# Optimization experiments

Measured on AMD Instinct MI355X. Metric: run time of the kernel, lower is better.

The kernel has to match this reference:

```python
import jax, jax.numpy as jnp
import numpy as np

BN_EPS = 1e-5


def setup_inputs() -> dict:
    key = jax.random.key(0)
    ks = jax.random.split(key, 10)
    B, C, L = 16, 512, 1024
    scale = 1.0 / np.sqrt(C)
    inp = {
        "x": jax.random.normal(ks[0], (B, C, L), dtype=jnp.float32),
        "gamma": jnp.ones((C,), jnp.float32),
        "beta": jnp.zeros((C,), jnp.float32),
        "Wq": jax.random.normal(ks[1], (C, C), jnp.float32) * scale,
        "bq": jnp.zeros((C,), jnp.float32),
        "Wk": jax.random.normal(ks[2], (C, C), jnp.float32) * scale,
        "bk": jnp.zeros((C,), jnp.float32),
        "Wv": jax.random.normal(ks[3], (C, C), jnp.float32) * scale,
        "bv": jnp.zeros((C,), jnp.float32),
        "Wp": jax.random.normal(ks[4], (C, C), jnp.float32) * scale,
        "bp": jnp.zeros((C,), jnp.float32),
    }
    return inp


def _pointwise(W, b, h):
    # Conv1d with kernel_size=1 == per-position linear: [C_out,C_in] x [B,C_in,L]
    return jnp.einsum("oc,bcl->bol", W, h) + b[None, :, None]


def reference(x, gamma, beta, Wq, bq, Wk, bk, Wv, bv, Wp, bp):
    B, C, L = x.shape
    # BatchNorm1d (training-mode batch statistics over batch & length dims)
    mean = jnp.mean(x, axis=(0, 2), keepdims=True)
    var = jnp.var(x, axis=(0, 2), keepdims=True)
    hn = (x - mean) * jax.lax.rsqrt(var + BN_EPS)
    hn = hn * gamma[None, :, None] + beta[None, :, None]

    q = _pointwise(Wq, bq, hn)  # [B,C,L]
    k = _pointwise(Wk, bk, hn)
    v = _pointwise(Wv, bv, hn)

    # attn[b,i,j] = sum_c q[b,c,i] k[b,c,j] / sqrt(C); i=query pos, j=key pos
    attn = jnp.einsum("bci,bcj->bij", q, k) * (C ** -0.5)
    attn = jax.nn.softmax(attn, axis=-1)

    # out[b,c,i] = sum_j attn[b,i,j] v[b,c,j]
    h_ = jnp.einsum("bij,bcj->bci", attn, v)
    h_ = _pointwise(Wp, bp, h_)
    return x + h_
```

## Files before the change

kernel.cpp:

```cpp
#include <hip/hip_runtime.h>
#include <hip/hip_bf16.h>


#define BB 16
#define CC 512
#define LL 1024

typedef __bf16 bf16x8 __attribute__((ext_vector_type(8)));
typedef float  f32x4  __attribute__((ext_vector_type(4)));

__device__ inline unsigned short bf16_bits(float f) {
  __hip_bfloat16 h = __float2bfloat16(f);
  return __builtin_bit_cast(unsigned short, h);
}
__device__ inline float bits_lo(unsigned int u) {
  return __builtin_bit_cast(float, u << 16);
}
__device__ inline float bits_hi(unsigned int u) {
  return __builtin_bit_cast(float, u & 0xffff0000u);
}

__global__ __launch_bounds__(256) void bn_stats(
    const float* __restrict__ x, const float* __restrict__ gamma,
    const float* __restrict__ beta, float* __restrict__ scl,
    float* __restrict__ sft) {
  int c = blockIdx.x;
  int t = threadIdx.x;
  float s = 0.f, s2 = 0.f;
  for (int b = 0; b < BB; ++b) {
    float4 v = ((const float4*)(x + ((size_t)(b * CC + c)) * LL))[t];
    s  += v.x + v.y + v.z + v.w;
    s2 += v.x * v.x + v.y * v.y + v.z * v.z + v.w * v.w;
  }
  for (int m = 32; m; m >>= 1) { s += __shfl_xor(s, m, 64); s2 += __shfl_xor(s2, m, 64); }
  __shared__ float rs[4], rs2[4];
  int wave = t >> 6, lane = t & 63;
  if (lane == 0) { rs[wave] = s; rs2[wave] = s2; }
  __syncthreads();
  if (t == 0) {
    float S  = rs[0] + rs[1] + rs[2] + rs[3];
    float S2 = rs2[0] + rs2[1] + rs2[2] + rs2[3];
    float mean = S * (1.f / 16384.f);
    float var  = S2 * (1.f / 16384.f) - mean * mean;
    float sc = gamma[c] * rsqrtf(var + 1e-5f);
    scl[c] = sc;
    sft[c] = beta[c] - mean * sc;
  }
}

__global__ __launch_bounds__(256) void cast4(
    const float* __restrict__ Wq, const float* __restrict__ Wk,
    const float* __restrict__ Wv, const float* __restrict__ Wp,
    __hip_bfloat16* __restrict__ Wqkv, __hip_bfloat16* __restrict__ Wpb) {
  int m = blockIdx.y;
  const float* src = m == 0 ? Wq : m == 1 ? Wk : m == 2 ? Wv : Wp;
  __hip_bfloat16* dst = m < 3 ? Wqkv + (size_t)m * 262144 : Wpb;
  int i = blockIdx.x * 256 + threadIdx.x;
  float4 v = ((const float4*)src)[i];
  ushort4 o;
  o.x = bf16_bits(v.x); o.y = bf16_bits(v.y);
  o.z = bf16_bits(v.z); o.w = bf16_bits(v.w);
  ((ushort4*)dst)[i] = o;
}

__global__ __launch_bounds__(256) void norm_t(
    const float* __restrict__ x, const float* __restrict__ scl,
    const float* __restrict__ sft, __hip_bfloat16* __restrict__ hnT) {
  __shared__ float tile[32][33];
  int l0 = blockIdx.x * 32, c0 = blockIdx.y * 32, b = blockIdx.z;
  int t = threadIdx.x;
#pragma unroll
  for (int i = 0; i < 4; ++i) {
    int idx = t + i * 256;
    int cc = idx >> 5, ll = idx & 31;
    tile[cc][ll] = x[((size_t)(b * CC + c0 + cc)) * LL + l0 + ll];
  }
  __syncthreads();
#pragma unroll
  for (int i = 0; i < 2; ++i) {
    int idx = t + i * 256;
    int ll = idx >> 4, cc = (idx & 15) * 2;
    float v0 = tile[cc][ll] * scl[c0 + cc] + sft[c0 + cc];
    float v1 = tile[cc + 1][ll] * scl[c0 + cc + 1] + sft[c0 + cc + 1];
    ushort2 o; o.x = bf16_bits(v0); o.y = bf16_bits(v1);
    *(ushort2*)(hnT + ((size_t)(b * LL + l0 + ll)) * CC + c0 + cc) = o;
  }
}

__global__ __launch_bounds__(256) void softmax_bf16(__hip_bfloat16* __restrict__ S) {
  int wave = threadIdx.x >> 6, lane = threadIdx.x & 63;
  size_t row = (size_t)blockIdx.x * 4 + wave;
  uint4* p = (uint4*)(S + row * 1024);
  uint4 r0 = p[lane * 2], r1 = p[lane * 2 + 1];
  float f[16];
  unsigned int w[8] = {r0.x, r0.y, r0.z, r0.w, r1.x, r1.y, r1.z, r1.w};
#pragma unroll
  for (int i = 0; i < 8; ++i) { f[2 * i] = bits_lo(w[i]); f[2 * i + 1] = bits_hi(w[i]); }
  float mx = f[0];
#pragma unroll
  for (int i = 1; i < 16; ++i) mx = fmaxf(mx, f[i]);
  for (int m = 32; m; m >>= 1) mx = fmaxf(mx, __shfl_xor(mx, m, 64));
  float s = 0.f;
#pragma unroll
  for (int i = 0; i < 16; ++i) { f[i] = __expf(f[i] - mx); s += f[i]; }
  for (int m = 32; m; m >>= 1) s += __shfl_xor(s, m, 64);
  float inv = 1.f / s;
  unsigned int ow[8];
#pragma unroll
  for (int i = 0; i < 8; ++i) {
    unsigned int lo = bf16_bits(f[2 * i] * inv);
    unsigned int hi = bf16_bits(f[2 * i + 1] * inv);
    ow[i] = lo | (hi << 16);
  }
  uint4 o0 = {ow[0], ow[1], ow[2], ow[3]}, o1 = {ow[4], ow[5], ow[6], ow[7]};
  p[lane * 2] = o0; p[lane * 2 + 1] = o1;
}

__device__ __forceinline__ void gemm_core(
    const __hip_bfloat16* __restrict__ A, int lda,
    const __hip_bfloat16* __restrict__ B, int ldb, int K,
    __hip_bfloat16* sA, __hip_bfloat16* sB, f32x4 (&acc)[4][4]) {
  const int tid = threadIdx.x;
  const int wave = tid >> 6, lane = tid & 63;
  const int wm = (wave >> 1) * 64, wn = (wave & 1) * 64;
  const int row0 = tid >> 2;
  const int ke0 = (((tid & 3) ^ ((tid >> 3) & 3)) * 8);
  const int fr = lane & 15;
  const int q = lane >> 4;
  const int colA = ((q ^ ((fr >> 1) & 3)) * 8);
  for (int k0 = 0; k0 < K; k0 += 32) {
    __syncthreads();
#pragma unroll
    for (int it = 0; it < 2; ++it) {
      const __hip_bfloat16* ga = A + (size_t)(it * 64 + row0) * lda + (k0 + ke0);
      const __hip_bfloat16* gb = B + (size_t)(it * 64 + row0) * ldb + (k0 + ke0);
      __builtin_amdgcn_global_load_lds(
          (__attribute__((address_space(1))) void*)(void*)ga,
          (__attribute__((address_space(3))) void*)(sA + (it * 256 + wave * 64) * 8),
          16, 0, 0);
      __builtin_amdgcn_global_load_lds(
          (__attribute__((address_space(1))) void*)(void*)gb,
          (__attribute__((address_space(3))) void*)(sB + (it * 256 + wave * 64) * 8),
          16, 0, 0);
    }
    __syncthreads();
    bf16x8 af[4], bfr[4];
#pragma unroll
    for (int i = 0; i < 4; ++i) {
      af[i]  = *(const bf16x8*)(sA + (wm + i * 16 + fr) * 32 + colA);
      bfr[i] = *(const bf16x8*)(sB + (wn + i * 16 + fr) * 32 + colA);
    }
#pragma unroll
    for (int i = 0; i < 4; ++i)
#pragma unroll
      for (int j = 0; j < 4; ++j)
        acc[i][j] = __builtin_amdgcn_mfma_f32_16x16x32_bf16(af[i], bfr[j], acc[i][j], 0, 0, 0);
  }
}

__global__ __launch_bounds__(256, 3) void gemm_qkv(
    const __hip_bfloat16* __restrict__ Wb, const __hip_bfloat16* __restrict__ hnT,
    __hip_bfloat16* __restrict__ qT, __hip_bfloat16* __restrict__ kT,
    __hip_bfloat16* __restrict__ vN,
    const float* __restrict__ bq, const float* __restrict__ bk,
    const float* __restrict__ bv) {
  __shared__ __align__(16) __hip_bfloat16 sA[128 * 32];
  __shared__ __align__(16) __hip_bfloat16 sB[128 * 32];
  const int bat = blockIdx.z;
  const int m0 = blockIdx.y * 128, n0 = blockIdx.x * 128;
  f32x4 acc[4][4] = {};
  gemm_core(Wb + (size_t)m0 * 512, 512,
            hnT + (size_t)bat * LL * CC + (size_t)n0 * 512, 512, 512, sA, sB, acc);
  const int lane = threadIdx.x & 63, wave = threadIdx.x >> 6;
  const int wm = (wave >> 1) * 64, wn = (wave & 1) * 64;
  const int crow = (lane >> 4) * 4, ccol = lane & 15;
  const int id = m0 >> 9;
  const int mloc0 = m0 & 511;
  const float* bias = id == 0 ? bq : id == 1 ? bk : bv;
  if (id < 2) {
    __hip_bfloat16* D = (id == 0 ? qT : kT) + (size_t)bat * LL * CC;
#pragma unroll
    for (int i = 0; i < 4; ++i) {
      int mg = mloc0 + wm + i * 16 + crow;
      float bv4[4];
#pragma unroll
      for (int r = 0; r < 4; ++r) bv4[r] = bias[mg + r];
#pragma unroll
      for (int j = 0; j < 4; ++j) {
        int ng = n0 + wn + j * 16 + ccol;
        ushort4 o;
        o.x = bf16_bits(acc[i][j][0] + bv4[0]);
        o.y = bf16_bits(acc[i][j][1] + bv4[1]);
        o.z = bf16_bits(acc[i][j][2] + bv4[2]);
        o.w = bf16_bits(acc[i][j][3] + bv4[3]);
        *(ushort4*)(D + (size_t)ng * 512 + mg) = o;
      }
    }
  } else {
    __hip_bfloat16* D = vN + (size_t)bat * CC * LL;
#pragma unroll
    for (int i = 0; i < 4; ++i) {
      int mg = mloc0 + wm + i * 16 + crow;
      float bv4[4];
#pragma unroll
      for (int r = 0; r < 4; ++r) bv4[r] = bias[mg + r];
#pragma unroll
      for (int j = 0; j < 4; ++j) {
        int ng = n0 + wn + j * 16 + ccol;
#pragma unroll
        for (int r = 0; r < 4; ++r)
          D[(size_t)(mg + r) * 1024 + ng] = __float2bfloat16(acc[i][j][r] + bv4[r]);
      }
    }
  }
}

template <int MODE, bool BIAS>
__global__ __launch_bounds__(256, 3) void gemm_tn(
    const __hip_bfloat16* __restrict__ A, int lda, size_t strideA,
    const __hip_bfloat16* __restrict__ B, int ldb, size_t strideB,
    void* __restrict__ Dp, int ldd, size_t strideD,
    const float* __restrict__ bias, float scale,
    const float* __restrict__ resid, size_t strideR, int K) {
  __shared__ __align__(16) __hip_bfloat16 sA[128 * 32];
  __shared__ __align__(16) __hip_bfloat16 sB[128 * 32];
  const int bat = blockIdx.z;
  const int m0 = blockIdx.y * 128, n0 = blockIdx.x * 128;
  f32x4 acc[4][4] = {};
  gemm_core(A + (size_t)bat * strideA + (size_t)m0 * lda, lda,
            B + (size_t)bat * strideB + (size_t)n0 * ldb, ldb, K, sA, sB, acc);
  const int lane = threadIdx.x & 63, wave = threadIdx.x >> 6;
  const int wm = (wave >> 1) * 64, wn = (wave & 1) * 64;
  const int crow = (lane >> 4) * 4, ccol = lane & 15;
  if constexpr (MODE == 0) {
    __hip_bfloat16* D = (__hip_bfloat16*)Dp + (size_t)bat * strideD;
#pragma unroll
    for (int i = 0; i < 4; ++i) {
      int mg = m0 + wm + i * 16 + crow;
      float bv4[4];
#pragma unroll
      for (int r = 0; r < 4; ++r) bv4[r] = BIAS ? bias[mg + r] : 0.f;
#pragma unroll
      for (int j = 0; j < 4; ++j) {
        int ng = n0 + wn + j * 16 + ccol;
#pragma unroll
        for (int r = 0; r < 4; ++r)
          D[(size_t)(mg + r) * ldd + ng] =
              __float2bfloat16(acc[i][j][r] * scale + bv4[r]);
      }
    }
  } else {
    float* D = (float*)Dp + (size_t)bat * strideD;
#pragma unroll
    for (int i = 0; i < 4; ++i) {
      int mg = m0 + wm + i * 16 + crow;
      float bv4[4];
#pragma unroll
      for (int r = 0; r < 4; ++r) bv4[r] = BIAS ? bias[mg + r] : 0.f;
#pragma unroll
      for (int j = 0; j < 4; ++j) {
        int ng = n0 + wn + j * 16 + ccol;
        const float* rsrc = resid + (size_t)bat * strideR + (size_t)mg * ldd + ng;
        float* dst = D + (size_t)mg * ldd + ng;
#pragma unroll
        for (int r = 0; r < 4; ++r)
          dst[(size_t)r * ldd] = acc[i][j][r] * scale + bv4[r] + rsrc[(size_t)r * ldd];
      }
    }
  }
}

extern "C" void kernel_launch(void* const* d_in, const int* in_sizes, int n_in,
                              void* d_out, int out_size, void* d_ws, size_t ws_size,
                              hipStream_t stream) {
  const float* x     = (const float*)d_in[0];
  const float* gamma = (const float*)d_in[1];
  const float* beta  = (const float*)d_in[2];
  const float* Wq    = (const float*)d_in[3];
  const float* bq    = (const float*)d_in[4];
  const float* Wk    = (const float*)d_in[5];
  const float* bk    = (const float*)d_in[6];
  const float* Wv    = (const float*)d_in[7];
  const float* bv    = (const float*)d_in[8];
  const float* Wp    = (const float*)d_in[9];
  const float* bp    = (const float*)d_in[10];
  float* out = (float*)d_out;

  char* ws = (char*)d_ws;
  float* scl = (float*)ws;
  float* sft = scl + 512;
  __hip_bfloat16* Wqkvb = (__hip_bfloat16*)(ws + 4096);
  __hip_bfloat16* Wpb = Wqkvb + 786432;
  __hip_bfloat16* hnT = Wpb + 262144;
  __hip_bfloat16* qT  = hnT + 8388608;
  __hip_bfloat16* kT  = qT + 8388608;
  __hip_bfloat16* vN  = kT + 8388608;
  __hip_bfloat16* Sb  = vN + 8388608;
  __hip_bfloat16* HT  = hnT;

  bn_stats<<<512, 256, 0, stream>>>(x, gamma, beta, scl, sft);
  cast4<<<dim3(256, 4), 256, 0, stream>>>(Wq, Wk, Wv, Wp, Wqkvb, Wpb);
  norm_t<<<dim3(32, 16, 16), 256, 0, stream>>>(x, scl, sft, hnT);

  const size_t sLC = (size_t)LL * CC;
  const size_t sCL = (size_t)CC * LL;
  const size_t sLLb = (size_t)LL * LL;

  gemm_qkv<<<dim3(8, 12, 16), 256, 0, stream>>>(Wqkvb, hnT, qT, kT, vN, bq, bk, bv);
  gemm_tn<0, false><<<dim3(8, 8, 16), 256, 0, stream>>>(
      qT, 512, sLC, kT, 512, sLC, Sb, 1024, sLLb, nullptr,
      0.04419417382415922f, nullptr, 0, 512);
  softmax_bf16<<<4096, 256, 0, stream>>>(Sb);
  gemm_tn<0, false><<<dim3(4, 8, 16), 256, 0, stream>>>(
      Sb, 1024, sLLb, vN, 1024, sCL, HT, 512, sLC, nullptr, 1.f, nullptr, 0, 1024);
  gemm_tn<3, true><<<dim3(8, 4, 16), 256, 0, stream>>>(
      Wpb, 512, 0, HT, 512, sLC, out, 1024, sCL, bp, 1.f, x, sCL, 512);
}
```

Before: 244.2 us.

## Triple-buffer GEMM LDS loads and swap operands for vectorized transposed epilogues

The shared GEMM core now uses a three-stage LDS ring buffer. Loads for tile k+2 are issued while tile k is computed, and partial vmcnt waits replace the two full barriers per K step. This hides global-load latency. The GEMMs also swap A/B operand roles (V projection, scores as K·Q, PV and output projection transposed) so every epilogue writes packed 4-wide bf16 or float4 vectors instead of scattered scalar stores. This costs 48KB of LDS per block, which may cut occupancy below the requested three blocks per CU, and the qkv kernel is split into separate qk and v launches.

```diff
diff --git a/kernel.cpp b/kernel.cpp
--- a/kernel.cpp
+++ b/kernel.cpp
@@ -51,10 +51,11 @@
 __global__ __launch_bounds__(256) void cast4(
     const float* __restrict__ Wq, const float* __restrict__ Wk,
     const float* __restrict__ Wv, const float* __restrict__ Wp,
-    __hip_bfloat16* __restrict__ Wqkv, __hip_bfloat16* __restrict__ Wpb) {
+    __hip_bfloat16* __restrict__ Wqk, __hip_bfloat16* __restrict__ Wvb,
+    __hip_bfloat16* __restrict__ Wpb) {
   int m = blockIdx.y;
   const float* src = m == 0 ? Wq : m == 1 ? Wk : m == 2 ? Wv : Wp;
-  __hip_bfloat16* dst = m < 3 ? Wqkv + (size_t)m * 262144 : Wpb;
+  __hip_bfloat16* dst = m == 0 ? Wqk : m == 1 ? Wqk + 262144 : m == 2 ? Wvb : Wpb;
   int i = blockIdx.x * 256 + threadIdx.x;
   float4 v = ((const float4*)src)[i];
   ushort4 o;
@@ -116,10 +117,16 @@
   p[lane * 2] = o0; p[lane * 2 + 1] = o1;
 }
 
+__device__ inline void glds(const __hip_bfloat16* g, __hip_bfloat16* l) {
+  __builtin_amdgcn_global_load_lds(
+      (__attribute__((address_space(1))) void*)(void*)g,
+      (__attribute__((address_space(3))) void*)l, 16, 0, 0);
+}
+
 __device__ __forceinline__ void gemm_core(
     const __hip_bfloat16* __restrict__ A, int lda,
     const __hip_bfloat16* __restrict__ B, int ldb, int K,
-    __hip_bfloat16* sA, __hip_bfloat16* sB, f32x4 (&acc)[4][4]) {
+    __hip_bfloat16* sm, f32x4 (&acc)[4][4]) {
   const int tid = threadIdx.x;
   const int wave = tid >> 6, lane = tid & 63;
   const int wm = (wave >> 1) * 64, wn = (wave & 1) * 64;
@@ -128,144 +135,147 @@
   const int fr = lane & 15;
   const int q = lane >> 4;
   const int colA = ((q ^ ((fr >> 1) & 3)) * 8);
-  for (int k0 = 0; k0 < K; k0 += 32) {
-    __syncthreads();
-#pragma unroll
-    for (int it = 0; it < 2; ++it) {
-      const __hip_bfloat16* ga = A + (size_t)(it * 64 + row0) * lda + (k0 + ke0);
-      const __hip_bfloat16* gb = B + (size_t)(it * 64 + row0) * ldb + (k0 + ke0);
-      __builtin_amdgcn_global_load_lds(
-          (__attribute__((address_space(1))) void*)(void*)ga,
-          (__attribute__((address_space(3))) void*)(sA + (it * 256 + wave * 64) * 8),
-          16, 0, 0);
-      __builtin_amdgcn_global_load_lds(
-          (__attribute__((address_space(1))) void*)(void*)gb,
-          (__attribute__((address_space(3))) void*)(sB + (it * 256 + wave * 64) * 8),
-          16, 0, 0);
-    }
-    __syncthreads();
+  const int dofs = wave * 512;
+
+  const __hip_bfloat16* ga0 = A + (size_t)row0 * lda + ke0;
+  const __hip_bfloat16* ga1 = ga0 + (size_t)64 * lda;
+  const __hip_bfloat16* gb0 = B + (size_t)row0 * ldb + ke0;
+  const __hip_bfloat16* gb1 = gb0 + (size_t)64 * ldb;
+
+  __hip_bfloat16* rb = sm;
+  __hip_bfloat16* nb = sm + 8192;
+  __hip_bfloat16* wb = sm + 16384;
+
+  const int niters = K >> 5;
+  {
+    glds(ga0, rb + dofs);          glds(ga1, rb + 2048 + dofs);
+    glds(gb0, rb + 4096 + dofs);   glds(gb1, rb + 6144 + dofs);
+    glds(ga0 + 32, nb + dofs);        glds(ga1 + 32, nb + 2048 + dofs);
+    glds(gb0 + 32, nb + 4096 + dofs); glds(gb1 + 32, nb + 6144 + dofs);
+  }
+  for (int k = 0; k < niters; ++k) {
+    if (k + 1 < niters) __builtin_amdgcn_s_waitcnt(0x0F74);
+    else                __builtin_amdgcn_s_waitcnt(0x0F70);
+    __builtin_amdgcn_s_barrier();
+    if (k + 2 < niters) {
+      int ko = (k + 2) * 32;
+      glds(ga0 + ko, wb + dofs);          glds(ga1 + ko, wb + 2048 + dofs);
+      glds(gb0 + ko, wb + 4096 + dofs);   glds(gb1 + ko, wb + 6144 + dofs);
+    }
     bf16x8 af[4], bfr[4];
 #pragma unroll
     for (int i = 0; i < 4; ++i) {
-      af[i]  = *(const bf16x8*)(sA + (wm + i * 16 + fr) * 32 + colA);
-      bfr[i] = *(const bf16x8*)(sB + (wn + i * 16 + fr) * 32 + colA);
+      af[i]  = *(const bf16x8*)(rb + (wm + i * 16 + fr) * 32 + colA);
+      bfr[i] = *(const bf16x8*)(rb + 4096 + (wn + i * 16 + fr) * 32 + colA);
     }
 #pragma unroll
     for (int i = 0; i < 4; ++i)
 #pragma unroll
       for (int j = 0; j < 4; ++j)
         acc[i][j] = __builtin_amdgcn_mfma_f32_16x16x32_bf16(af[i], bfr[j], acc[i][j], 0, 0, 0);
-  }
-}
-
-__global__ __launch_bounds__(256, 3) void gemm_qkv(
+    __hip_bfloat16* t = rb; rb = nb; nb = wb; wb = t;
+  }
+}
+
+__global__ __launch_bounds__(256, 3) void gemm_qk(
     const __hip_bfloat16* __restrict__ Wb, const __hip_bfloat16* __restrict__ hnT,
     __hip_bfloat16* __restrict__ qT, __hip_bfloat16* __restrict__ kT,
-    __hip_bfloat16* __restrict__ vN,
-    const float* __restrict__ bq, const float* __restrict__ bk,
-    const float* __restrict__ bv) {
-  __shared__ __align__(16) __hip_bfloat16 sA[128 * 32];
-  __shared__ __align__(16) __hip_bfloat16 sB[128 * 32];
+    const float* __restrict__ bq, const float* __restrict__ bk) {
+  __shared__ __align__(16) __hip_bfloat16 sm[3 * 8192];
   const int bat = blockIdx.z;
   const int m0 = blockIdx.y * 128, n0 = blockIdx.x * 128;
   f32x4 acc[4][4] = {};
   gemm_core(Wb + (size_t)m0 * 512, 512,
-            hnT + (size_t)bat * LL * CC + (size_t)n0 * 512, 512, 512, sA, sB, acc);
+            hnT + (size_t)bat * LL * CC + (size_t)n0 * 512, 512, 512, sm, acc);
   const int lane = threadIdx.x & 63, wave = threadIdx.x >> 6;
   const int wm = (wave >> 1) * 64, wn = (wave & 1) * 64;
   const int crow = (lane >> 4) * 4, ccol = lane & 15;
   const int id = m0 >> 9;
   const int mloc0 = m0 & 511;
-  const float* bias = id == 0 ? bq : id == 1 ? bk : bv;
-  if (id < 2) {
-    __hip_bfloat16* D = (id == 0 ? qT : kT) + (size_t)bat * LL * CC;
-#pragma unroll
-    for (int i = 0; i < 4; ++i) {
-      int mg = mloc0 + wm + i * 16 + crow;
-      float bv4[4];
-#pragma unroll
-      for (int r = 0; r < 4; ++r) bv4[r] = bias[mg + r];
-#pragma unroll
-      for (int j = 0; j < 4; ++j) {
-        int ng = n0 + wn + j * 16 + ccol;
-        ushort4 o;
-        o.x = bf16_bits(acc[i][j][0] + bv4[0]);
-        o.y = bf16_bits(acc[i][j][1] + bv4[1]);
-        o.z = bf16_bits(acc[i][j][2] + bv4[2]);
-        o.w = bf16_bits(acc[i][j][3] + bv4[3]);
-        *(ushort4*)(D + (size_t)ng * 512 + mg) = o;
-      }
-    }
-  } else {
-    __hip_bfloat16* D = vN + (size_t)bat * CC * LL;
-#pragma unroll
-    for (int i = 0; i < 4; ++i) {
-      int mg = mloc0 + wm + i * 16 + crow;
-      float bv4[4];
-#pragma unroll
-      for (int r = 0; r < 4; ++r) bv4[r] = bias[mg + r];
-#pragma unroll
-      for (int j = 0; j < 4; ++j) {
-        int ng = n0 + wn + j * 16 + ccol;
-#pragma unroll
-        for (int r = 0; r < 4; ++r)
-          D[(size_t)(mg + r) * 1024 + ng] = __float2bfloat16(acc[i][j][r] + bv4[r]);
-      }
-    }
-  }
-}
-
-template <int MODE, bool BIAS>
-__global__ __launch_bounds__(256, 3) void gemm_tn(
+  const float* bias = id == 0 ? bq : bk;
+  __hip_bfloat16* D = (id == 0 ? qT : kT) + (size_t)bat * LL * CC;
+#pragma unroll
+  for (int i = 0; i < 4; ++i) {
+    int mg = mloc0 + wm + i * 16 + crow;
+    float bv4[4];
+#pragma unroll
+    for (int r = 0; r < 4; ++r) bv4[r] = bias[mg + r];
+#pragma unroll
+    for (int j = 0; j < 4; ++j) {
+      int ng = n0 + wn + j * 16 + ccol;
+      ushort4 o;
+      o.x = bf16_bits(acc[i][j][0] + bv4[0]);
+      o.y = bf16_bits(acc[i][j][1] + bv4[1]);
+      o.z = bf16_bits(acc[i][j][2] + bv4[2]);
+      o.w = bf16_bits(acc[i][j][3] + bv4[3]);
+      *(ushort4*)(D + (size_t)ng * 512 + mg) = o;
+    }
+  }
+}
+
+template <bool BIAS>
+__global__ __launch_bounds__(256, 3) void gemm_bf16t(
     const __hip_bfloat16* __restrict__ A, int lda, size_t strideA,
     const __hip_bfloat16* __restrict__ B, int ldb, size_t strideB,
-    void* __restrict__ Dp, int ldd, size_t strideD,
-    const float* __restrict__ bias, float scale,
-    const float* __restrict__ resid, size_t strideR, int K) {
-  __shared__ __align__(16) __hip_bfloat16 sA[128 * 32];
-  __shared__ __align__(16) __hip_bfloat16 sB[128 * 32];
+    __hip_bfloat16* __restrict__ D, int ldd, size_t strideD,
+    const float* __restrict__ bias, float scale, int K) {
+  __shared__ __align__(16) __hip_bfloat16 sm[3 * 8192];
   const int bat = blockIdx.z;
   const int m0 = blockIdx.y * 128, n0 = blockIdx.x * 128;
   f32x4 acc[4][4] = {};
   gemm_core(A + (size_t)bat * strideA + (size_t)m0 * lda, lda,
-            B + (size_t)bat * strideB + (size_t)n0 * ldb, ldb, K, sA, sB, acc);
+            B + (size_t)bat * strideB + (size_t)n0 * ldb, ldb, K, sm, acc);
   const int lane = threadIdx.x & 63, wave = threadIdx.x >> 6;
   const int wm = (wave >> 1) * 64, wn = (wave & 1) * 64;
   const int crow = (lane >> 4) * 4, ccol = lane & 15;
-  if constexpr (MODE == 0) {
-    __hip_bfloat16* D = (__hip_bfloat16*)Dp + (size_t)bat * strideD;
+  __hip_bfloat16* Db = D + (size_t)bat * strideD;
+#pragma unroll
+  for (int j = 0; j < 4; ++j) {
+    int ng = n0 + wn + j * 16 + ccol;
+    float bn = BIAS ? bias[ng] : 0.f;
 #pragma unroll
     for (int i = 0; i < 4; ++i) {
       int mg = m0 + wm + i * 16 + crow;
-      float bv4[4];
-#pragma unroll
-      for (int r = 0; r < 4; ++r) bv4[r] = BIAS ? bias[mg + r] : 0.f;
-#pragma unroll
-      for (int j = 0; j < 4; ++j) {
-        int ng = n0 + wn + j * 16 + ccol;
-#pragma unroll
-        for (int r = 0; r < 4; ++r)
-          D[(size_t)(mg + r) * ldd + ng] =
-              __float2bfloat16(acc[i][j][r] * scale + bv4[r]);
-      }
-    }
-  } else {
-    float* D = (float*)Dp + (size_t)bat * strideD;
+      ushort4 o;
+      o.x = bf16_bits(acc[i][j][0] * scale + bn);
+      o.y = bf16_bits(acc[i][j][1] * scale + bn);
+      o.z = bf16_bits(acc[i][j][2] * scale + bn);
+      o.w = bf16_bits(acc[i][j][3] * scale + bn);
+      *(ushort4*)(Db + (size_t)ng * ldd + mg) = o;
+    }
+  }
+}
+
+__global__ __launch_bounds__(256, 3) void gemm_f32t(
+    const __hip_bfloat16* __restrict__ A, int lda, size_t strideA,
+    const __hip_bfloat16* __restrict__ B, int ldb,
+    float* __restrict__ D, int ldd, size_t strideD,
+    const float* __restrict__ bias, const float* __restrict__ resid, int K) {
+  __shared__ __align__(16) __hip_bfloat16 sm[3 * 8192];
+  const int bat = blockIdx.z;
+  const int m0 = blockIdx.y * 128, n0 = blockIdx.x * 128;
+  f32x4 acc[4][4] = {};
+  gemm_core(A + (size_t)bat * strideA + (size_t)m0 * lda, lda,
+            B + (size_t)n0 * ldb, ldb, K, sm, acc);
+  const int lane = threadIdx.x & 63, wave = threadIdx.x >> 6;
+  const int wm = (wave >> 1) * 64, wn = (wave & 1) * 64;
+  const int crow = (lane >> 4) * 4, ccol = lane & 15;
+  float* Db = D + (size_t)bat * strideD;
+  const float* Rb = resid + (size_t)bat * strideD;
+#pragma unroll
+  for (int j = 0; j < 4; ++j) {
+    int ng = n0 + wn + j * 16 + ccol;
+    float bn = bias[ng];
 #pragma unroll
     for (int i = 0; i < 4; ++i) {
       int mg = m0 + wm + i * 16 + crow;
-      float bv4[4];
-#pragma unroll
-      for (int r = 0; r < 4; ++r) bv4[r] = BIAS ? bias[mg + r] : 0.f;
-#pragma unroll
-      for (int j = 0; j < 4; ++j) {
-        int ng = n0 + wn + j * 16 + ccol;
-        const float* rsrc = resid + (size_t)bat * strideR + (size_t)mg * ldd + ng;
-        float* dst = D + (size_t)mg * ldd + ng;
-#pragma unroll
-        for (int r = 0; r < 4; ++r)
-          dst[(size_t)r * ldd] = acc[i][j][r] * scale + bv4[r] + rsrc[(size_t)r * ldd];
-      }
+      float4 r = *(const float4*)(Rb + (size_t)ng * ldd + mg);
+      float4 o;
+      o.x = acc[i][j][0] + bn + r.x;
+      o.y = acc[i][j][1] + bn + r.y;
+      o.z = acc[i][j][2] + bn + r.z;
+      o.w = acc[i][j][3] + bn + r.w;
+      *(float4*)(Db + (size_t)ng * ldd + mg) = o;
     }
   }
 }
@@ -289,30 +299,33 @@
   char* ws = (char*)d_ws;
   float* scl = (float*)ws;
   float* sft = scl + 512;
-  __hip_bfloat16* Wqkvb = (__hip_bfloat16*)(ws + 4096);
-  __hip_bfloat16* Wpb = Wqkvb + 786432;
-  __hip_bfloat16* hnT = Wpb + 262144;
-  __hip_bfloat16* qT  = hnT + 8388608;
-  __hip_bfloat16* kT  = qT + 8388608;
-  __hip_bfloat16* vN  = kT + 8388608;
-  __hip_bfloat16* Sb  = vN + 8388608;
-  __hip_bfloat16* HT  = hnT;
-
-  bn_stats<<<512, 256, 0, stream>>>(x, gamma, beta, scl, sft);
-  cast4<<<dim3(256, 4), 256, 0, stream>>>(Wq, Wk, Wv, Wp, Wqkvb, Wpb);
-  norm_t<<<dim3(32, 16, 16), 256, 0, stream>>>(x, scl, sft, hnT);
+  __hip_bfloat16* Wqkb = (__hip_bfloat16*)(ws + 4096);
+  __hip_bfloat16* Wvb  = Wqkb + 524288;
+  __hip_bfloat16* Wpb  = Wvb + 262144;
+  __hip_bfloat16* hnT  = Wpb + 262144;
+  __hip_bfloat16* qT   = hnT + 8388608;
+  __hip_bfloat16* kT   = qT + 8388608;
+  __hip_bfloat16* vN   = kT + 8388608;
+  __hip_bfloat16* Sb   = vN + 8388608;
+  __hip_bfloat16* HT   = hnT;
 
   const size_t sLC = (size_t)LL * CC;
   const size_t sCL = (size_t)CC * LL;
   const size_t sLLb = (size_t)LL * LL;
 
-  gemm_qkv<<<dim3(8, 12, 16), 256, 0, stream>>>(Wqkvb, hnT, qT, kT, vN, bq, bk, bv);
-  gemm_tn<0, false><<<dim3(8, 8, 16), 256, 0, stream>>>(
-      qT, 512, sLC, kT, 512, sLC, Sb, 1024, sLLb, nullptr,
-      0.04419417382415922f, nullptr, 0, 512);
+  bn_stats<<<512, 256, 0, stream>>>(x, gamma, beta, scl, sft);
+  cast4<<<dim3(256, 4), 256, 0, stream>>>(Wq, Wk, Wv, Wp, Wqkb, Wvb, Wpb);
+  norm_t<<<dim3(32, 16, 16), 256, 0, stream>>>(x, scl, sft, hnT);
+
+  gemm_qk<<<dim3(8, 8, 16), 256, 0, stream>>>(Wqkb, hnT, qT, kT, bq, bk);
+  gemm_bf16t<true><<<dim3(4, 8, 16), 256, 0, stream>>>(
+      hnT, 512, sLC, Wvb, 512, 0, vN, 1024, sCL, bv, 1.f, 512);
+  gemm_bf16t<false><<<dim3(8, 8, 16), 256, 0, stream>>>(
+      kT, 512, sLC, qT, 512, sLC, Sb, 1024, sLLb, nullptr,
+      0.04419417382415922f, 512);
   softmax_bf16<<<4096, 256, 0, stream>>>(Sb);
-  gemm_tn<0, false><<<dim3(4, 8, 16), 256, 0, stream>>>(
-      Sb, 1024, sLLb, vN, 1024, sCL, HT, 512, sLC, nullptr, 1.f, nullptr, 0, 1024);
-  gemm_tn<3, true><<<dim3(8, 4, 16), 256, 0, stream>>>(
-      Wpb, 512, 0, HT, 512, sLC, out, 1024, sCL, bp, 1.f, x, sCL, 512);
-}
+  gemm_bf16t<false><<<dim3(8, 4, 16), 256, 0, stream>>>(
+      vN, 1024, sCL, Sb, 1024, sLLb, HT, 512, sLC, nullptr, 1.f, 1024);
+  gemm_f32t<<<dim3(4, 8, 16), 256, 0, stream>>>(
+      HT, 512, sLC, Wpb, 512, out, 1024, sCL, bp, x, 512);
+}
```

Measured after the change: 254.5 us. 1.04x slower.

## Fuse softmax normalization into PV GEMM and transpose epilogues for vector stores

Applied to the files above, without the earlier changes.

The softmax pass now only computes per-row max and inverse sum and writes them to a small stats buffer, instead of rewriting the full score matrix. The P·V GEMM recomputes exp(s-max)*inv on the fly while loading score tiles, which removes one full read-write of the score matrix. The S and output-projection GEMMs swap operand roles so epilogues write 4-wide vectorized stores along the contiguous dimension. The cost is extra exp work inside the GEMM inner loop, repeated for each of the four channel tiles.

```diff
diff --git a/kernel.cpp b/kernel.cpp
--- a/kernel.cpp
+++ b/kernel.cpp
@@ -87,10 +87,11 @@
   }
 }
 
-__global__ __launch_bounds__(256) void softmax_bf16(__hip_bfloat16* __restrict__ S) {
+__global__ __launch_bounds__(256) void row_stats(
+    const __hip_bfloat16* __restrict__ S, float2* __restrict__ st) {
   int wave = threadIdx.x >> 6, lane = threadIdx.x & 63;
   size_t row = (size_t)blockIdx.x * 4 + wave;
-  uint4* p = (uint4*)(S + row * 1024);
+  const uint4* p = (const uint4*)(S + row * 1024);
   uint4 r0 = p[lane * 2], r1 = p[lane * 2 + 1];
   float f[16];
   unsigned int w[8] = {r0.x, r0.y, r0.z, r0.w, r1.x, r1.y, r1.z, r1.w};
@@ -102,18 +103,15 @@
   for (int m = 32; m; m >>= 1) mx = fmaxf(mx, __shfl_xor(mx, m, 64));
   float s = 0.f;
 #pragma unroll
-  for (int i = 0; i < 16; ++i) { f[i] = __expf(f[i] - mx); s += f[i]; }
+  for (int i = 0; i < 16; ++i) s += __expf(f[i] - mx);
   for (int m = 32; m; m >>= 1) s += __shfl_xor(s, m, 64);
-  float inv = 1.f / s;
-  unsigned int ow[8];
-#pragma unroll
-  for (int i = 0; i < 8; ++i) {
-    unsigned int lo = bf16_bits(f[2 * i] * inv);
-    unsigned int hi = bf16_bits(f[2 * i + 1] * inv);
-    ow[i] = lo | (hi << 16);
-  }
-  uint4 o0 = {ow[0], ow[1], ow[2], ow[3]}, o1 = {ow[4], ow[5], ow[6], ow[7]};
-  p[lane * 2] = o0; p[lane * 2 + 1] = o1;
+  if (lane == 0) st[row] = make_float2(mx, 1.f / s);
+}
+
+__device__ inline void glds(const __hip_bfloat16* g, __hip_bfloat16* l) {
+  __builtin_amdgcn_global_load_lds(
+      (__attribute__((address_space(1))) void*)(void*)g,
+      (__attribute__((address_space(3))) void*)l, 16, 0, 0);
 }
 
 __device__ __forceinline__ void gemm_core(
@@ -134,14 +132,8 @@
     for (int it = 0; it < 2; ++it) {
       const __hip_bfloat16* ga = A + (size_t)(it * 64 + row0) * lda + (k0 + ke0);
       const __hip_bfloat16* gb = B + (size_t)(it * 64 + row0) * ldb + (k0 + ke0);
-      __builtin_amdgcn_global_load_lds(
-          (__attribute__((address_space(1))) void*)(void*)ga,
-          (__attribute__((address_space(3))) void*)(sA + (it * 256 + wave * 64) * 8),
-          16, 0, 0);
-      __builtin_amdgcn_global_load_lds(
-          (__attribute__((address_space(1))) void*)(void*)gb,
-          (__attribute__((address_space(3))) void*)(sB + (it * 256 + wave * 64) * 8),
-          16, 0, 0);
+      glds(ga, sA + (it * 256 + wave * 64) * 8);
+      glds(gb, sB + (it * 256 + wave * 64) * 8);
     }
     __syncthreads();
     bf16x8 af[4], bfr[4];
@@ -215,57 +207,142 @@
   }
 }
 
-template <int MODE, bool BIAS>
-__global__ __launch_bounds__(256, 3) void gemm_tn(
+__global__ __launch_bounds__(256, 3) void gemm_s(
+    const __hip_bfloat16* __restrict__ kT, const __hip_bfloat16* __restrict__ qT,
+    __hip_bfloat16* __restrict__ Sb) {
+  __shared__ __align__(16) __hip_bfloat16 sA[128 * 32];
+  __shared__ __align__(16) __hip_bfloat16 sB[128 * 32];
+  const int bat = blockIdx.z;
+  const int m0 = blockIdx.y * 128, n0 = blockIdx.x * 128;
+  f32x4 acc[4][4] = {};
+  const size_t sLC = (size_t)LL * CC;
+  gemm_core(kT + (size_t)bat * sLC + (size_t)m0 * 512, 512,
+            qT + (size_t)bat * sLC + (size_t)n0 * 512, 512, 512, sA, sB, acc);
+  const int lane = threadIdx.x & 63, wave = threadIdx.x >> 6;
+  const int wm = (wave >> 1) * 64, wn = (wave & 1) * 64;
+  const int crow = (lane >> 4) * 4, ccol = lane & 15;
+  const float scale = 0.04419417382415922f;
+  __hip_bfloat16* Db = Sb + (size_t)bat * LL * LL;
+#pragma unroll
+  for (int j = 0; j < 4; ++j) {
+    int ng = n0 + wn + j * 16 + ccol;
+#pragma unroll
+    for (int i = 0; i < 4; ++i) {
+      int mg = m0 + wm + i * 16 + crow;
+      ushort4 o;
+      o.x = bf16_bits(acc[i][j][0] * scale);
+      o.y = bf16_bits(acc[i][j][1] * scale);
+      o.z = bf16_bits(acc[i][j][2] * scale);
+      o.w = bf16_bits(acc[i][j][3] * scale);
+      *(ushort4*)(Db + (size_t)ng * 1024 + mg) = o;
+    }
+  }
+}
+
+__global__ __launch_bounds__(256, 3) void attn_pv(
+    const __hip_bfloat16* __restrict__ vN, const __hip_bfloat16* __restrict__ Sb,
+    const float2* __restrict__ st, __hip_bfloat16* __restrict__ HT) {
+  __shared__ __align__(16) __hip_bfloat16 sA[128 * 32];
+  __shared__ __align__(16) __hip_bfloat16 sB[128 * 32];
+  __shared__ float sM[128], sLi[128];
+  const int bat = blockIdx.z;
+  const int m0 = blockIdx.y * 128;
+  const int n0 = blockIdx.x * 128;
+  const int tid = threadIdx.x;
+  if (tid < 128) {
+    float2 s = st[(size_t)bat * LL + n0 + tid];
+    sM[tid] = s.x; sLi[tid] = s.y;
+  }
+  const __hip_bfloat16* A = vN + (size_t)bat * CC * LL + (size_t)m0 * 1024;
+  const __hip_bfloat16* B = Sb + (size_t)bat * LL * LL + (size_t)n0 * 1024;
+  const int wave = tid >> 6, lane = tid & 63;
+  const int wm = (wave >> 1) * 64, wn = (wave & 1) * 64;
+  const int row0 = tid >> 2;
+  const int ke0 = (((tid & 3) ^ ((tid >> 3) & 3)) * 8);
+  const int fr = lane & 15;
+  const int q = lane >> 4;
+  const int colA = ((q ^ ((fr >> 1) & 3)) * 8);
+  f32x4 acc[4][4] = {};
+  for (int k0 = 0; k0 < 1024; k0 += 32) {
+    __syncthreads();
+#pragma unroll
+    for (int it = 0; it < 2; ++it) {
+      glds(A + (size_t)(it * 64 + row0) * 1024 + (k0 + ke0),
+           sA + (it * 256 + wave * 64) * 8);
+      glds(B + (size_t)(it * 64 + row0) * 1024 + (k0 + ke0),
+           sB + (it * 256 + wave * 64) * 8);
+    }
+    __syncthreads();
+    bf16x8 af[4], bfr[4];
+#pragma unroll
+    for (int i = 0; i < 4; ++i)
+      af[i] = *(const bf16x8*)(sA + (wm + i * 16 + fr) * 32 + colA);
+#pragma unroll
+    for (int j = 0; j < 4; ++j) {
+      int rrow = wn + j * 16 + fr;
+      float mrow = sM[rrow], li = sLi[rrow];
+      bf16x8 raw = *(const bf16x8*)(sB + rrow * 32 + colA);
+      bf16x8 p;
+#pragma unroll
+      for (int e = 0; e < 8; ++e)
+        p[e] = (__bf16)(__expf((float)raw[e] - mrow) * li);
+      bfr[j] = p;
+    }
+#pragma unroll
+    for (int i = 0; i < 4; ++i)
+#pragma unroll
+      for (int j = 0; j < 4; ++j)
+        acc[i][j] = __builtin_amdgcn_mfma_f32_16x16x32_bf16(af[i], bfr[j], acc[i][j], 0, 0, 0);
+  }
+  const int crow = (lane >> 4) * 4, ccol = lane & 15;
+  __hip_bfloat16* Db = HT + (size_t)bat * LL * CC;
+#pragma unroll
+  for (int j = 0; j < 4; ++j) {
+    int ng = n0 + wn + j * 16 + ccol;
+#pragma unroll
+    for (int i = 0; i < 4; ++i) {
+      int mg = m0 + wm + i * 16 + crow;
+      ushort4 o;
+      o.x = bf16_bits(acc[i][j][0]);
+      o.y = bf16_bits(acc[i][j][1]);
+      o.z = bf16_bits(acc[i][j][2]);
+      o.w = bf16_bits(acc[i][j][3]);
+      *(ushort4*)(Db + (size_t)ng * 512 + mg) = o;
+    }
+  }
+}
+
+__global__ __launch_bounds__(256, 3) void gemm_f32t(
     const __hip_bfloat16* __restrict__ A, int lda, size_t strideA,
-    const __hip_bfloat16* __restrict__ B, int ldb, size_t strideB,
-    void* __restrict__ Dp, int ldd, size_t strideD,
-    const float* __restrict__ bias, float scale,
-    const float* __restrict__ resid, size_t strideR, int K) {
+    const __hip_bfloat16* __restrict__ B, int ldb,
+    float* __restrict__ D, int ldd, size_t strideD,
+    const float* __restrict__ bias, const float* __restrict__ resid, int K) {
   __shared__ __align__(16) __hip_bfloat16 sA[128 * 32];
   __shared__ __align__(16) __hip_bfloat16 sB[128 * 32];
   const int bat = blockIdx.z;
   const int m0 = blockIdx.y * 128, n0 = blockIdx.x * 128;
   f32x4 acc[4][4] = {};
   gemm_core(A + (size_t)bat * strideA + (size_t)m0 * lda, lda,
-            B + (size_t)bat * strideB + (size_t)n0 * ldb, ldb, K, sA, sB, acc);
+            B + (size_t)n0 * ldb, ldb, K, sA, sB, acc);
   const int lane = threadIdx.x & 63, wave = threadIdx.x >> 6;
   const int wm = (wave >> 1) * 64, wn = (wave & 1) * 64;
   const int crow = (lane >> 4) * 4, ccol = lane & 15;
-  if constexpr (MODE == 0) {
-    __hip_bfloat16* D = (__hip_bfloat16*)Dp + (size_t)bat * strideD;
+  float* Db = D + (size_t)bat * strideD;
+  const float* Rb = resid + (size_t)bat * strideD;
+#pragma unroll
+  for (int j = 0; j < 4; ++j) {
+    int ng = n0 + wn + j * 16 + ccol;
+    float bn = bias[ng];
 #pragma unroll
     for (int i = 0; i < 4; ++i) {
       int mg = m0 + wm + i * 16 + crow;
-      float bv4[4];
-#pragma unroll
-      for (int r = 0; r < 4; ++r) bv4[r] = BIAS ? bias[mg + r] : 0.f;
-#pragma unroll
-      for (int j = 0; j < 4; ++j) {
-        int ng = n0 + wn + j * 16 + ccol;
-#pragma unroll
-        for (int r = 0; r < 4; ++r)
-          D[(size_t)(mg + r) * ldd + ng] =
-              __float2bfloat16(acc[i][j][r] * scale + bv4[r]);
-      }
-    }
-  } else {
-    float* D = (float*)Dp + (size_t)bat * strideD;
-#pragma unroll
-    for (int i = 0; i < 4; ++i) {
-      int mg = m0 + wm + i * 16 + crow;
-      float bv4[4];
-#pragma unroll
-      for (int r = 0; r < 4; ++r) bv4[r] = BIAS ? bias[mg + r] : 0.f;
-#pragma unroll
-      for (int j = 0; j < 4; ++j) {
-        int ng = n0 + wn + j * 16 + ccol;
-        const float* rsrc = resid + (size_t)bat * strideR + (size_t)mg * ldd + ng;
-        float* dst = D + (size_t)mg * ldd + ng;
-#pragma unroll
-        for (int r = 0; r < 4; ++r)
-          dst[(size_t)r * ldd] = acc[i][j][r] * scale + bv4[r] + rsrc[(size_t)r * ldd];
-      }
+      float4 r = *(const float4*)(Rb + (size_t)ng * ldd + mg);
+      float4 o;
+      o.x = acc[i][j][0] + bn + r.x;
+      o.y = acc[i][j][1] + bn + r.y;
+      o.z = acc[i][j][2] + bn + r.z;
+      o.w = acc[i][j][3] + bn + r.w;
+      *(float4*)(Db + (size_t)ng * ldd + mg) = o;
     }
   }
 }
@@ -290,29 +367,26 @@
   float* scl = (float*)ws;
   float* sft = scl + 512;
   __hip_bfloat16* Wqkvb = (__hip_bfloat16*)(ws + 4096);
-  __hip_bfloat16* Wpb = Wqkvb + 786432;
-  __hip_bfloat16* hnT = Wpb + 262144;
-  __hip_bfloat16* qT  = hnT + 8388608;
-  __hip_bfloat16* kT  = qT + 8388608;
-  __hip_bfloat16* vN  = kT + 8388608;
-  __hip_bfloat16* Sb  = vN + 8388608;
-  __hip_bfloat16* HT  = hnT;
+  __hip_bfloat16* Wpb  = Wqkvb + 786432;
+  __hip_bfloat16* hnT  = Wpb + 262144;
+  __hip_bfloat16* qT   = hnT + 8388608;
+  __hip_bfloat16* kT   = qT + 8388608;
+  __hip_bfloat16* vN   = kT + 8388608;
+  __hip_bfloat16* Sb   = vN + 8388608;
+  float2* stats = (float2*)(Sb + 16777216);
+  __hip_bfloat16* HT   = hnT;
+
+  const size_t sLC = (size_t)LL * CC;
+  const size_t sCL = (size_t)CC * LL;
 
   bn_stats<<<512, 256, 0, stream>>>(x, gamma, beta, scl, sft);
   cast4<<<dim3(256, 4), 256, 0, stream>>>(Wq, Wk, Wv, Wp, Wqkvb, Wpb);
   norm_t<<<dim3(32, 16, 16), 256, 0, stream>>>(x, scl, sft, hnT);
 
-  const size_t sLC = (size_t)LL * CC;
-  const size_t sCL = (size_t)CC * LL;
-  const size_t sLLb = (size_t)LL * LL;
-
   gemm_qkv<<<dim3(8, 12, 16), 256, 0, stream>>>(Wqkvb, hnT, qT, kT, vN, bq, bk, bv);
-  gemm_tn<0, false><<<dim3(8, 8, 16), 256, 0, stream>>>(
-      qT, 512, sLC, kT, 512, sLC, Sb, 1024, sLLb, nullptr,
-      0.04419417382415922f, nullptr, 0, 512);
-  softmax_bf16<<<4096, 256, 0, stream>>>(Sb);
-  gemm_tn<0, false><<<dim3(4, 8, 16), 256, 0, stream>>>(
-      Sb, 1024, sLLb, vN, 1024, sCL, HT, 512, sLC, nullptr, 1.f, nullptr, 0, 1024);
-  gemm_tn<3, true><<<dim3(8, 4, 16), 256, 0, stream>>>(
-      Wpb, 512, 0, HT, 512, sLC, out, 1024, sCL, bp, 1.f, x, sCL, 512);
-}
+  gemm_s<<<dim3(8, 8, 16), 256, 0, stream>>>(kT, qT, Sb);
+  row_stats<<<4096, 256, 0, stream>>>(Sb, stats);
+  attn_pv<<<dim3(8, 4, 16), 256, 0, stream>>>(vN, Sb, stats, HT);
+  gemm_f32t<<<dim3(4, 8, 16), 256, 0, stream>>>(
+      HT, 512, sLC, Wpb, 512, out, 1024, sCL, bp, x, 512);
+}
```

After: 264.5 us. 1.08x slower.
